# Optimization experiments

Measured on AMD Instinct MI355X. Metric: run time of the kernel, lower is better.

## Reference

```python
import jax, jax.numpy as jnp
import numpy as np

NH = 16      # num_heads
EPS = 1e-6   # RMSNorm eps


def rmsnorm(x, w):
    return x * jax.lax.rsqrt(jnp.mean(x * x, axis=-1, keepdims=True) + EPS) * w


def rotate_half(x):
    x1, x2 = jnp.split(x, 2, axis=-1)
    return jnp.concatenate([-x2, x1], axis=-1)


def apply_rope(x, cos, sin):
    # x: [B,H,N,hd]; cos/sin: [N,hd]
    return x * cos + rotate_half(x) * sin


def attention(x, qkv_w, qkv_b, qn_w, kn_w, proj_w, proj_b, cos, sin):
    B, N, C = x.shape
    hd = C // NH
    qkv = (x @ qkv_w.T + qkv_b).reshape(B, N, 3, NH, hd).transpose(2, 0, 3, 1, 4)
    q, k, v = qkv[0], qkv[1], qkv[2]            # [B,H,N,hd]
    q = apply_rope(rmsnorm(q, qn_w), cos, sin)
    k = apply_rope(rmsnorm(k, kn_w), cos, sin)
    scores = jnp.einsum('bhqd,bhkd->bhqk', q, k) / jnp.sqrt(jnp.float32(hd))
    attn = jax.nn.softmax(scores, axis=-1)
    out = jnp.einsum('bhqk,bhkd->bhqd', attn, v)
    out = out.transpose(0, 2, 1, 3).reshape(B, N, C)
    return out @ proj_w.T + proj_b


def jit_block(x, c, cos_s, sin_s, cos_t, sin_t,
              norm1_w, norm2_w, norm3_w,
              qkv_s_w, qkv_s_b, qn_s_w, kn_s_w, proj_s_w, proj_s_b,
              qkv_t_w, qkv_t_b, qn_t_w, kn_t_w, proj_t_w, proj_t_b,
              w12_w, w12_b, w3_w, w3_b, ada_w, ada_b):
    B, T, L, D = x.shape
    mods = (jax.nn.silu(c) @ ada_w.T + ada_b).reshape(B, 9, D)
    sh_s, sc_s, g_s = mods[:, 0], mods[:, 1], mods[:, 2]
    sh_t, sc_t, g_t = mods[:, 3], mods[:, 4], mods[:, 5]
    sh_m, sc_m, g_m = mods[:, 6], mods[:, 7], mods[:, 8]

    # spatial attention over L, batched over B*T
    xs = x.reshape(B * T, L, D)
    sh = jnp.repeat(sh_s, T, axis=0)
    sc = jnp.repeat(sc_s, T, axis=0)
    g = jnp.repeat(g_s, T, axis=0)
    xs_n = rmsnorm(xs, norm1_w) * (1 + sc[:, None, :]) + sh[:, None, :]
    xs = xs + g[:, None, :] * attention(xs_n, qkv_s_w, qkv_s_b, qn_s_w, kn_s_w,
                                        proj_s_w, proj_s_b, cos_s, sin_s)
    x = xs.reshape(B, T, L, D)

    # temporal attention over T, batched over B*L
    xt = x.transpose(0, 2, 1, 3).reshape(B * L, T, D)
    sh = jnp.repeat(sh_t, L, axis=0)
    sc = jnp.repeat(sc_t, L, axis=0)
    g = jnp.repeat(g_t, L, axis=0)
    xt_n = rmsnorm(xt, norm2_w) * (1 + sc[:, None, :]) + sh[:, None, :]
    xt = xt + g[:, None, :] * attention(xt_n, qkv_t_w, qkv_t_b, qn_t_w, kn_t_w,
                                        proj_t_w, proj_t_b, cos_t, sin_t)
    x = xt.reshape(B, L, T, D).transpose(0, 2, 1, 3)

    # SwiGLU FFN with adaLN modulation + gate
    x_n = rmsnorm(x, norm3_w) * (1 + sc_m[:, None, None, :]) + sh_m[:, None, None, :]
    h12 = x_n @ w12_w.T + w12_b
    h1, h2 = jnp.split(h12, 2, axis=-1)
    mlp_out = (jax.nn.silu(h1) * h2) @ w3_w.T + w3_b
    return x + g_m[:, None, None, :] * mlp_out


def _rope_tables(n, hd):
    inv = 1.0 / (10000.0 ** (np.arange(0, hd, 2, dtype=np.float64) / hd))
    ang = np.arange(n, dtype=np.float64)[:, None] * inv[None, :]
    cos = np.concatenate([np.cos(ang), np.cos(ang)], -1).astype(np.float32)
    sin = np.concatenate([np.sin(ang), np.sin(ang)], -1).astype(np.float32)
    return jnp.asarray(cos), jnp.asarray(sin)


def setup_inputs() -> dict:
    key = jax.random.key(0)
    B, T, L, D = 2, 16, 256, 1024
    HD = D // NH
    HFF = int(int(D * 4.0) * 2 / 3)  # 2730
    ks = jax.random.split(key, 16)
    s = 0.02
    cos_s, sin_s = _rope_tables(L, HD)
    cos_t, sin_t = _rope_tables(T, HD)
    return {
        'x': jax.random.normal(ks[0], (B, T, L, D), jnp.float32),
        'c': jax.random.normal(ks[1], (B, D), jnp.float32),
        'cos_s': cos_s, 'sin_s': sin_s, 'cos_t': cos_t, 'sin_t': sin_t,
        'norm1_w': jnp.ones((D,), jnp.float32),
        'norm2_w': jnp.ones((D,), jnp.float32),
        'norm3_w': jnp.ones((D,), jnp.float32),
        'qkv_s_w': jax.random.normal(ks[2], (3 * D, D), jnp.float32) * s,
        'qkv_s_b': jnp.zeros((3 * D,), jnp.float32),
        'qn_s_w': jnp.ones((HD,), jnp.float32),
        'kn_s_w': jnp.ones((HD,), jnp.float32),
        'proj_s_w': jax.random.normal(ks[3], (D, D), jnp.float32) * s,
        'proj_s_b': jnp.zeros((D,), jnp.float32),
        'qkv_t_w': jax.random.normal(ks[4], (3 * D, D), jnp.float32) * s,
        'qkv_t_b': jnp.zeros((3 * D,), jnp.float32),
        'qn_t_w': jnp.ones((HD,), jnp.float32),
        'kn_t_w': jnp.ones((HD,), jnp.float32),
        'proj_t_w': jax.random.normal(ks[5], (D, D), jnp.float32) * s,
        'proj_t_b': jnp.zeros((D,), jnp.float32),
        'w12_w': jax.random.normal(ks[6], (2 * HFF, D), jnp.float32) * s,
        'w12_b': jnp.zeros((2 * HFF,), jnp.float32),
        'w3_w': jax.random.normal(ks[7], (D, HFF), jnp.float32) * s,
        'w3_b': jnp.zeros((D,), jnp.float32),
        'ada_w': jax.random.normal(ks[8], (9 * D, D), jnp.float32) * s,
        'ada_b': jnp.zeros((9 * D,), jnp.float32),
    }


def reference(x, c, cos_s, sin_s, cos_t, sin_t,
              norm1_w, norm2_w, norm3_w,
              qkv_s_w, qkv_s_b, qn_s_w, kn_s_w, proj_s_w, proj_s_b,
              qkv_t_w, qkv_t_b, qn_t_w, kn_t_w, proj_t_w, proj_t_b,
              w12_w, w12_b, w3_w, w3_b, ada_w, ada_b):
    return jit_block(x, c, cos_s, sin_s, cos_t, sin_t,
                     norm1_w, norm2_w, norm3_w,
                     qkv_s_w, qkv_s_b, qn_s_w, kn_s_w, proj_s_w, proj_s_b,
                     qkv_t_w, qkv_t_b, qn_t_w, kn_t_w, proj_t_w, proj_t_b,
                     w12_w, w12_b, w3_w, w3_b, ada_w, ada_b)
```

## Files before the change

kernel.cpp:

```cpp
#include <hip/hip_runtime.h>
#include <cstdint>
#include <cstddef>

typedef unsigned short u16;
typedef __attribute__((ext_vector_type(8))) short short8;
typedef __attribute__((ext_vector_type(4))) float f32x4;

__device__ __forceinline__ float bf2f(u16 u) {
  union { uint32_t u; float f; } x; x.u = ((uint32_t)u) << 16; return x.f;
}
__device__ __forceinline__ u16 f2bf(float f) {
  union { float f; uint32_t u; } x; x.f = f;
  uint32_t r = x.u + 0x7FFFu + ((x.u >> 16) & 1u);
  return (u16)(r >> 16);
}
__device__ __forceinline__ float silu_f(float x) { return x / (1.f + __expf(-x)); }

__device__ __forceinline__ void glds16(const u16* g, u16* l) {
  __builtin_amdgcn_global_load_lds(
      (const __attribute__((address_space(1))) void*)g,
      (__attribute__((address_space(3))) void*)l, 16, 0, 0);
}

#define MFMA16 __builtin_amdgcn_mfma_f32_16x16x32_bf16

__device__ __forceinline__ void wg_barrier() {
  __builtin_amdgcn_sched_barrier(0);
  asm volatile("" ::: "memory");
  __builtin_amdgcn_s_barrier();
  asm volatile("" ::: "memory");
  __builtin_amdgcn_sched_barrier(0);
}

__device__ __forceinline__ void swizzle_mn(int nx, int& mt, int& nt) {
  int bid = blockIdx.y * nx + blockIdx.x;
  int xcd = bid & 7, l = bid >> 3;
  nt = l >> 3;
  mt = (xcd << 3) | (l & 7);
}

__global__ void cvt_pad_kernel(const float* __restrict__ in, u16* __restrict__ out,
                               int cols_out, int rows_in, int cols_in, int row_off, int total) {
  int i = blockIdx.x * 256 + threadIdx.x;
  if (i >= total) return;
  int r = i / cols_out, ci = i - r * cols_out;
  float v = 0.f;
  if (r < rows_in && ci < cols_in) v = in[(size_t)(r + row_off) * cols_in + ci];
  out[i] = f2bf(v);
}

__global__ void mods_kernel(const float* __restrict__ c, const float* __restrict__ ada_w,
                            const float* __restrict__ ada_b, float* __restrict__ mods) {
  int j = blockIdx.x * 4 + (threadIdx.x >> 6);
  int lane = threadIdx.x & 63;
  float a0 = 0.f, a1 = 0.f;
  for (int k = lane; k < 1024; k += 64) {
    float w = ada_w[(size_t)j * 1024 + k];
    a0 += silu_f(c[k]) * w;
    a1 += silu_f(c[1024 + k]) * w;
  }
  #pragma unroll
  for (int off = 32; off > 0; off >>= 1) { a0 += __shfl_down(a0, off); a1 += __shfl_down(a1, off); }
  if (lane == 0) {
    float bb = ada_b[j];
    mods[j] = a0 + bb;
    mods[9216 + j] = a1 + bb;
  }
}

__global__ __launch_bounds__(256) void norm_mod_kernel(
    const float* __restrict__ X, u16* __restrict__ Y,
    const float* __restrict__ nw, const float* __restrict__ mods,
    int sh_idx, int transpose) {
  int row = blockIdx.x;
  int b = row >> 12;
  int in_row;
  if (transpose) { int rem = row & 4095; int l = rem >> 4, t = rem & 15; in_row = (b << 12) + (t << 8) + l; }
  else in_row = row;
  int tid = threadIdx.x;
  float4 v = ((const float4*)(X + (size_t)in_row * 1024))[tid];
  float ss = v.x * v.x + v.y * v.y + v.z * v.z + v.w * v.w;
  #pragma unroll
  for (int off = 32; off > 0; off >>= 1) ss += __shfl_down(ss, off);
  __shared__ float red[4];
  if ((tid & 63) == 0) red[tid >> 6] = ss;
  __syncthreads();
  float rms = rsqrtf((red[0] + red[1] + red[2] + red[3]) * (1.f / 1024.f) + 1e-6f);
  const float* mb = mods + (size_t)b * 9216 + (size_t)sh_idx * 1024;
  float4 sh = ((const float4*)mb)[tid];
  float4 sc = ((const float4*)(mb + 1024))[tid];
  float4 w  = ((const float4*)nw)[tid];
  ushort4 o;
  o.x = f2bf(v.x * rms * w.x * (1.f + sc.x) + sh.x);
  o.y = f2bf(v.y * rms * w.y * (1.f + sc.y) + sh.y);
  o.z = f2bf(v.z * rms * w.z * (1.f + sc.z) + sh.z);
  o.w = f2bf(v.w * rms * w.w * (1.f + sc.w) + sh.w);
  ((ushort4*)(Y + (size_t)row * 1024))[tid] = o;
}

#define CHK2(b, s) (((b) * 4 + (s)) << 13)

__device__ __forceinline__ void stage_half(const u16* __restrict__ gp, int ldk,
                                           int row_base, int k0,
                                           u16* Sbase, int slot_u16,
                                           int wid, int srow, int scol) {
  #pragma unroll
  for (int c = 0; c < 2; c++) {
    int row = c * 64 + wid * 8 + srow;
    glds16(gp + (size_t)(row_base + row) * ldk + (k0 + scol),
           Sbase + slot_u16 + c * 4096 + wid * 512);
  }
}

template<int STORE_BF16>
__global__ __launch_bounds__(512, 2) void gemm256_bt(
    const u16* __restrict__ A, const u16* __restrict__ W,
    const float* __restrict__ bias, void* __restrict__ Cv,
    int K, int ldc) {
  __shared__ u16 S[65536];
  const int tid = threadIdx.x, wid = tid >> 6, lane = tid & 63;
  const int wm = wid >> 2, wn = wid & 3;
  const int quad = lane >> 4, r = lane & 15;
  const int bid = blockIdx.x, xcd = bid & 7, l = bid >> 3;
  const int mt = (xcd << 2) | (l & 3), nt = l >> 2;
  const int m0 = mt * 256, n0 = nt * 256;

  const int srow = lane >> 3;
  const int scol = ((lane & 7) ^ srow) << 3;
  const int kx0 = (quad * 8) ^ ((r & 7) << 3);
  const int kx1 = (32 + quad * 8) ^ ((r & 7) << 3);
  const int arow = (wm * 64 + r) * 64;
  const int brow = (wn * 32 + r) * 64;

  f32x4 zero = {0.f, 0.f, 0.f, 0.f};
  f32x4 acc[8][4];
  #pragma unroll
  for (int i = 0; i < 8; i++)
    #pragma unroll
    for (int j = 0; j < 4; j++) acc[i][j] = zero;
  short8 fA[4][2], fB0[2][2], fB1[2][2];

  const int nk = K >> 6;

  stage_half(A, K, m0,       0, S, CHK2(0,0), wid, srow, scol);
  stage_half(A, K, m0 + 128, 0, S, CHK2(0,1), wid, srow, scol);
  stage_half(W, K, n0,       0, S, CHK2(0,2), wid, srow, scol);
  stage_half(W, K, n0 + 128, 0, S, CHK2(0,3), wid, srow, scol);
  if (nk > 1) {
    stage_half(A, K, m0,       64, S, CHK2(1,0), wid, srow, scol);
    stage_half(W, K, n0 + 128, 64, S, CHK2(1,3), wid, srow, scol);
    asm volatile("s_waitcnt vmcnt(4)" ::: "memory");
  } else {
    asm volatile("s_waitcnt vmcnt(0)" ::: "memory");
  }
  __builtin_amdgcn_s_barrier();

  for (int u = 0; u < nk; ++u) {
    const int cur = u & 1, nxt = cur ^ 1;
    const int k1 = (u + 1) << 6, k2 = (u + 2) << 6;
    const int s1 = (u + 1 < nk), s2 = (u + 2 < nk);
    const u16* cA0 = S + CHK2(cur, 0);
    const u16* cA1 = S + CHK2(cur, 1);
    const u16* cB0 = S + CHK2(cur, 2);
    const u16* cB1 = S + CHK2(cur, 3);

    #pragma unroll
    for (int f = 0; f < 4; f++) {
      fA[f][0] = *(const short8*)(cA0 + arow + f * 1024 + kx0);
      fA[f][1] = *(const short8*)(cA0 + arow + f * 1024 + kx1);
    }
    #pragma unroll
    for (int j = 0; j < 2; j++) {
      fB0[j][0] = *(const short8*)(cB0 + brow + j * 1024 + kx0);
      fB0[j][1] = *(const short8*)(cB0 + brow + j * 1024 + kx1);
    }
    if (s1) stage_half(A, K, m0 + 128, k1, S, CHK2(nxt,1), wid, srow, scol);
    wg_barrier();
    __builtin_amdgcn_s_setprio(1);
    #pragma unroll
    for (int f = 0; f < 4; f++)
      #pragma unroll
      for (int j = 0; j < 2; j++) {
        acc[f][j] = MFMA16(fA[f][0], fB0[j][0], acc[f][j], 0, 0, 0);
        acc[f][j] = MFMA16(fA[f][1], fB0[j][1], acc[f][j], 0, 0, 0);
      }
    __builtin_amdgcn_s_setprio(0);
    wg_barrier();

    #pragma unroll
    for (int j = 0; j < 2; j++) {
      fB1[j][0] = *(const short8*)(cB1 + brow + j * 1024 + kx0);
      fB1[j][1] = *(const short8*)(cB1 + brow + j * 1024 + kx1);
    }
    if (s1) stage_half(W, K, n0, k1, S, CHK2(nxt,2), wid, srow, scol);
    wg_barrier();
    __builtin_amdgcn_s_setprio(1);
    #pragma unroll
    for (int f = 0; f < 4; f++)
      #pragma unroll
      for (int j = 0; j < 2; j++) {
        acc[f][2 + j] = MFMA16(fA[f][0], fB1[j][0], acc[f][2 + j], 0, 0, 0);
        acc[f][2 + j] = MFMA16(fA[f][1], fB1[j][1], acc[f][2 + j], 0, 0, 0);
      }
    __builtin_amdgcn_s_setprio(0);
    wg_barrier();

    #pragma unroll
    for (int f = 0; f < 4; f++) {
      fA[f][0] = *(const short8*)(cA1 + arow + f * 1024 + kx0);
      fA[f][1] = *(const short8*)(cA1 + arow + f * 1024 + kx1);
    }
    if (s2) stage_half(A, K, m0, k2, S, CHK2(cur,0), wid, srow, scol);
    wg_barrier();
    __builtin_amdgcn_s_setprio(1);
    #pragma unroll
    for (int f = 0; f < 4; f++)
      #pragma unroll
      for (int j = 0; j < 2; j++) {
        acc[4 + f][2 + j] = MFMA16(fA[f][0], fB1[j][0], acc[4 + f][2 + j], 0, 0, 0);
        acc[4 + f][2 + j] = MFMA16(fA[f][1], fB1[j][1], acc[4 + f][2 + j], 0, 0, 0);
      }
    __builtin_amdgcn_s_setprio(0);
    wg_barrier();

    if (s2) stage_half(W, K, n0 + 128, k2, S, CHK2(cur,3), wid, srow, scol);
    wg_barrier();
    __builtin_amdgcn_s_setprio(1);
    #pragma unroll
    for (int f = 0; f < 4; f++)
      #pragma unroll
      for (int j = 0; j < 2; j++) {
        acc[4 + f][j] = MFMA16(fA[f][0], fB0[j][0], acc[4 + f][j], 0, 0, 0);
        acc[4 + f][j] = MFMA16(fA[f][1], fB0[j][1], acc[4 + f][j], 0, 0, 0);
      }
    __builtin_amdgcn_s_setprio(0);
    __builtin_amdgcn_sched_barrier(0);
    if (s2)      asm volatile("s_waitcnt vmcnt(4)" ::: "memory");
    else if (s1) asm volatile("s_waitcnt vmcnt(0)" ::: "memory");
    wg_barrier();
  }

  float* Cf = (float*)Cv;
  u16* Ch = (u16*)Cv;
  #pragma unroll
  for (int f = 0; f < 8; f++) {
    int row = m0 + (f >> 2) * 128 + wm * 64 + (f & 3) * 16 + quad * 4;
    #pragma unroll
    for (int j = 0; j < 4; j++) {
      int col = n0 + (j >> 1) * 128 + wn * 32 + (j & 1) * 16 + r;
      float bv = bias[col];
      #pragma unroll
      for (int rr = 0; rr < 4; rr++) {
        float vv = acc[f][j][rr] + bv;
        if (STORE_BF16) Ch[(size_t)(row + rr) * ldc + col] = f2bf(vv);
        else            Cf[(size_t)(row + rr) * ldc + col] = vv;
      }
    }
  }
}

__global__ __launch_bounds__(512, 2) void gemm256_w12(
    const u16* __restrict__ A, const u16* __restrict__ W1, const u16* __restrict__ W2,
    const float* __restrict__ bias, u16* __restrict__ Hb) {
  __shared__ u16 S[65536];
  const int tid = threadIdx.x, wid = tid >> 6, lane = tid & 63;
  const int wm = wid >> 2, wn = wid & 3;
  const int quad = lane >> 4, r = lane & 15;
  const int bid = blockIdx.x, xcd = bid & 7, l = bid >> 3;
  const int mt = (xcd << 2) | (l & 3), nt = l >> 2;
  const int m0 = mt * 256, n0 = nt * 128;

  const int srow = lane >> 3;
  const int scol = ((lane & 7) ^ srow) << 3;
  const int kx0 = (quad * 8) ^ ((r & 7) << 3);
  const int kx1 = (32 + quad * 8) ^ ((r & 7) << 3);
  const int arow = (wm * 64 + r) * 64;
  const int brow = (wn * 32 + r) * 64;
  const int K = 1024, nk = 16;

  f32x4 zero = {0.f, 0.f, 0.f, 0.f};
  f32x4 acc1[8][2], acc2[8][2];
  #pragma unroll
  for (int i = 0; i < 8; i++)
    #pragma unroll
    for (int j = 0; j < 2; j++) { acc1[i][j] = zero; acc2[i][j] = zero; }
  short8 fA[4][2], fW1[2][2], fW2[2][2];

  stage_half(A,  K, m0,       0, S, CHK2(0,0), wid, srow, scol);
  stage_half(A,  K, m0 + 128, 0, S, CHK2(0,1), wid, srow, scol);
  stage_half(W1, K, n0,       0, S, CHK2(0,2), wid, srow, scol);
  stage_half(W2, K, n0,       0, S, CHK2(0,3), wid, srow, scol);
  stage_half(A,  K, m0,      64, S, CHK2(1,0), wid, srow, scol);
  stage_half(W2, K, n0,      64, S, CHK2(1,3), wid, srow, scol);
  asm volatile("s_waitcnt vmcnt(4)" ::: "memory");
  __builtin_amdgcn_s_barrier();

  for (int u = 0; u < nk; ++u) {
    const int cur = u & 1, nxt = cur ^ 1;
    const int k1 = (u + 1) << 6, k2 = (u + 2) << 6;
    const int s1 = (u + 1 < nk), s2 = (u + 2 < nk);
    const u16* cA0 = S + CHK2(cur, 0);
    const u16* cA1 = S + CHK2(cur, 1);
    const u16* cW1 = S + CHK2(cur, 2);
    const u16* cW2 = S + CHK2(cur, 3);

    #pragma unroll
    for (int f = 0; f < 4; f++) {
      fA[f][0] = *(const short8*)(cA0 + arow + f * 1024 + kx0);
      fA[f][1] = *(const short8*)(cA0 + arow + f * 1024 + kx1);
    }
    #pragma unroll
    for (int j = 0; j < 2; j++) {
      fW1[j][0] = *(const short8*)(cW1 + brow + j * 1024 + kx0);
      fW1[j][1] = *(const short8*)(cW1 + brow + j * 1024 + kx1);
    }
    if (s1) stage_half(A, K, m0 + 128, k1, S, CHK2(nxt,1), wid, srow, scol);
    wg_barrier();
    __builtin_amdgcn_s_setprio(1);
    #pragma unroll
    for (int f = 0; f < 4; f++)
      #pragma unroll
      for (int j = 0; j < 2; j++) {
        acc1[f][j] = MFMA16(fA[f][0], fW1[j][0], acc1[f][j], 0, 0, 0);
        acc1[f][j] = MFMA16(fA[f][1], fW1[j][1], acc1[f][j], 0, 0, 0);
      }
    __builtin_amdgcn_s_setprio(0);
    wg_barrier();

    #pragma unroll
    for (int j = 0; j < 2; j++) {
      fW2[j][0] = *(const short8*)(cW2 + brow + j * 1024 + kx0);
      fW2[j][1] = *(const short8*)(cW2 + brow + j * 1024 + kx1);
    }
    if (s1) stage_half(W1, K, n0, k1, S, CHK2(nxt,2), wid, srow, scol);
    wg_barrier();
    __builtin_amdgcn_s_setprio(1);
    #pragma unroll
    for (int f = 0; f < 4; f++)
      #pragma unroll
      for (int j = 0; j < 2; j++) {
        acc2[f][j] = MFMA16(fA[f][0], fW2[j][0], acc2[f][j], 0, 0, 0);
        acc2[f][j] = MFMA16(fA[f][1], fW2[j][1], acc2[f][j], 0, 0, 0);
      }
    __builtin_amdgcn_s_setprio(0);
    wg_barrier();

    #pragma unroll
    for (int f = 0; f < 4; f++) {
      fA[f][0] = *(const short8*)(cA1 + arow + f * 1024 + kx0);
      fA[f][1] = *(const short8*)(cA1 + arow + f * 1024 + kx1);
    }
    if (s2) stage_half(A, K, m0, k2, S, CHK2(cur,0), wid, srow, scol);
    wg_barrier();
    __builtin_amdgcn_s_setprio(1);
    #pragma unroll
    for (int f = 0; f < 4; f++)
      #pragma unroll
      for (int j = 0; j < 2; j++) {
        acc2[4 + f][j] = MFMA16(fA[f][0], fW2[j][0], acc2[4 + f][j], 0, 0, 0);
        acc2[4 + f][j] = MFMA16(fA[f][1], fW2[j][1], acc2[4 + f][j], 0, 0, 0);
      }
    __builtin_amdgcn_s_setprio(0);
    wg_barrier();

    if (s2) stage_half(W2, K, n0, k2, S, CHK2(cur,3), wid, srow, scol);
    wg_barrier();
    __builtin_amdgcn_s_setprio(1);
    #pragma unroll
    for (int f = 0; f < 4; f++)
      #pragma unroll
      for (int j = 0; j < 2; j++) {
        acc1[4 + f][j] = MFMA16(fA[f][0], fW1[j][0], acc1[4 + f][j], 0, 0, 0);
        acc1[4 + f][j] = MFMA16(fA[f][1], fW1[j][1], acc1[4 + f][j], 0, 0, 0);
      }
    __builtin_amdgcn_s_setprio(0);
    __builtin_amdgcn_sched_barrier(0);
    if (s2)      asm volatile("s_waitcnt vmcnt(4)" ::: "memory");
    else if (s1) asm volatile("s_waitcnt vmcnt(0)" ::: "memory");
    wg_barrier();
  }

  #pragma unroll
  for (int f = 0; f < 8; f++) {
    int row = m0 + (f >> 2) * 128 + wm * 64 + (f & 3) * 16 + quad * 4;
    #pragma unroll
    for (int j = 0; j < 2; j++) {
      int col = n0 + wn * 32 + j * 16 + r;
      float b1 = (col < 2730) ? bias[col] : 0.f;
      float b2 = (col < 2730) ? bias[2730 + col] : 0.f;
      #pragma unroll
      for (int rr = 0; rr < 4; rr++) {
        float h1 = acc1[f][j][rr] + b1;
        float h2 = acc2[f][j][rr] + b2;
        Hb[(size_t)(row + rr) * 2816 + col] = f2bf(silu_f(h1) * h2);
      }
    }
  }
}

template<int STORE_BF16>
__global__ __launch_bounds__(256) void gemm_bt(
    const u16* __restrict__ A, const u16* __restrict__ W,
    const float* __restrict__ bias, void* __restrict__ Cv,
    int N, int K, int ldc) {
  __shared__ u16 As[128 * 32];
  __shared__ u16 Bs[128 * 32];
  int tid = threadIdx.x;
  int wid = tid >> 6, lane = tid & 63;
  int quad = lane >> 4, r = lane & 15;
  int mt, nt; swizzle_mn(gridDim.x, mt, nt);
  int m0 = mt * 128, n0 = nt * 128;
  int wm = (wid >> 1) * 64, wn = (wid & 1) * 64;
  int crow = lane >> 2, ccol = (lane & 3) * 8;

  f32x4 zero = {0.f, 0.f, 0.f, 0.f};
  f32x4 acc[4][4];
  #pragma unroll
  for (int i = 0; i < 4; i++)
    #pragma unroll
    for (int j = 0; j < 4; j++) acc[i][j] = zero;

  for (int k0 = 0; k0 < K; k0 += 32) {
    #pragma unroll
    for (int half = 0; half < 2; half++) {
      int chunk = wid + half * 4;
      int row = chunk * 16 + crow;
      glds16(A + (size_t)(m0 + row) * K + k0 + ccol, As + chunk * 512);
      glds16(W + (size_t)(n0 + row) * K + k0 + ccol, Bs + chunk * 512);
    }
    __syncthreads();
    short8 afr[4], bfr[4];
    #pragma unroll
    for (int i = 0; i < 4; i++) afr[i] = *(const short8*)(As + (wm + i * 16 + r) * 32 + quad * 8);
    #pragma unroll
    for (int j = 0; j < 4; j++) bfr[j] = *(const short8*)(Bs + (wn + j * 16 + r) * 32 + quad * 8);
    #pragma unroll
    for (int i = 0; i < 4; i++)
      #pragma unroll
      for (int j = 0; j < 4; j++)
        acc[i][j] = MFMA16(afr[i], bfr[j], acc[i][j], 0, 0, 0);
    __syncthreads();
  }

  float* Cf = (float*)Cv;
  u16* Ch = (u16*)Cv;
  #pragma unroll
  for (int i = 0; i < 4; i++) {
    #pragma unroll
    for (int j = 0; j < 4; j++) {
      int col = n0 + wn + j * 16 + r;
      float bv = bias[col];
      #pragma unroll
      for (int rr = 0; rr < 4; rr++) {
        int row = m0 + wm + i * 16 + quad * 4 + rr;
        float vv = acc[i][j][rr] + bv;
        if (STORE_BF16) Ch[(size_t)row * ldc + col] = f2bf(vv);
        else            Cf[(size_t)row * ldc + col] = vv;
      }
    }
  }
}

#define KSS 72
#define VSS 264
#define PSS 40
__global__ __launch_bounds__(256) void attn_s_mfma(
    const u16* __restrict__ QKV,
    const float* __restrict__ qn_w, const float* __restrict__ kn_w,
    const float* __restrict__ cosT, const float* __restrict__ sinT,
    u16* __restrict__ AO) {
  __shared__ u16 Ks[256 * KSS];
  __shared__ u16 Vt[64 * VSS];
  __shared__ u16 Pl[4 * 32 * PSS];
  int pair = blockIdx.x;
  int s = pair >> 4, h = pair & 15;
  int qhalf = blockIdx.y;
  int tid = threadIdx.x, wid = tid >> 6, lane = tid & 63;
  int quad = lane >> 4, r = lane & 15;

  {
    int j = tid;
    size_t rowb = ((size_t)(s * 256 + j)) * 3072 + (size_t)h * 64;
    const short8* kr = (const short8*)(QKV + rowb + 1024);
    float xk[64]; float ssq = 0.f;
    #pragma unroll
    for (int cg = 0; cg < 8; cg++) {
      short8 kk = kr[cg];
      #pragma unroll
      for (int e = 0; e < 8; e++) { float v = bf2f((u16)kk[e]); xk[cg * 8 + e] = v; ssq += v * v; }
    }
    float rms = rsqrtf(ssq * (1.f / 64.f) + 1e-6f);
    short8 kq[8];
    #pragma unroll
    for (int d = 0; d < 32; d++) {
      float a = xk[d] * rms * kn_w[d];
      float b2 = xk[d + 32] * rms * kn_w[d + 32];
      u16 o0 = f2bf(a * cosT[j * 64 + d] - b2 * sinT[j * 64 + d]);
      u16 o1 = f2bf(b2 * cosT[j * 64 + 32 + d] + a * sinT[j * 64 + 32 + d]);
      kq[d >> 3][d & 7] = (short)o0;
      kq[(d + 32) >> 3][d & 7] = (short)o1;
    }
    #pragma unroll
    for (int cg = 0; cg < 8; cg++) *(short8*)(Ks + j * KSS + cg * 8) = kq[cg];
    const short8* vr = (const short8*)(QKV + rowb + 2048);
    #pragma unroll
    for (int cg = 0; cg < 8; cg++) {
      short8 vv = vr[cg];
      #pragma unroll
      for (int e = 0; e < 8; e++) Vt[(cg * 8 + e) * VSS + j] = (u16)vv[e];
    }
  }

  int qbase = qhalf * 128 + wid * 32;
  short8 qa[2][2];
  float lrow[2][4];
  {
    float qv[2][2][8];
    float ssq[2] = {0.f, 0.f};
    #pragma unroll
    for (int i = 0; i < 2; i++) {
      int grow = s * 256 + qbase + i * 16 + r;
      #pragma unroll
      for (int kk = 0; kk < 2; kk++) {
        short8 qraw = *(const short8*)(QKV + (size_t)grow * 3072 + h * 64 + kk * 32 + quad * 8);
        #pragma unroll
        for (int e = 0; e < 8; e++) { float v = bf2f((u16)qraw[e]); qv[i][kk][e] = v; ssq[i] += v * v; }
      }
    }
    #pragma unroll
    for (int i = 0; i < 2; i++) {
      float sv = ssq[i];
      sv += __shfl_xor(sv, 16);
      sv += __shfl_xor(sv, 32);
      float rms = rsqrtf(sv * (1.f / 64.f) + 1e-6f);
      int qrow = qbase + i * 16 + r;
      #pragma unroll
      for (int e = 0; e < 8; e++) {
        int d0 = quad * 8 + e;
        float a = qv[i][0][e] * rms * qn_w[d0];
        float b2 = qv[i][1][e] * rms * qn_w[d0 + 32];
        qa[i][0][e] = (short)f2bf(a * cosT[qrow * 64 + d0] - b2 * sinT[qrow * 64 + d0]);
        qa[i][1][e] = (short)f2bf(b2 * cosT[qrow * 64 + 32 + d0] + a * sinT[qrow * 64 + 32 + d0]);
      }
    }
  }
  __syncthreads();

  f32x4 zero = {0.f, 0.f, 0.f, 0.f};
  f32x4 acc[2][16];
  #pragma unroll
  for (int i = 0; i < 2; i++)
    #pragma unroll
    for (int j = 0; j < 16; j++) acc[i][j] = zero;
  #pragma unroll
  for (int kk = 0; kk < 2; kk++) {
    #pragma unroll
    for (int j = 0; j < 16; j++) {
      short8 bfr = *(const short8*)(Ks + (j * 16 + r) * KSS + kk * 32 + quad * 8);
      acc[0][j] = MFMA16(qa[0][kk], bfr, acc[0][j], 0, 0, 0);
      acc[1][j] = MFMA16(qa[1][kk], bfr, acc[1][j], 0, 0, 0);
    }
  }

  #pragma unroll
  for (int i = 0; i < 2; i++) {
    #pragma unroll
    for (int rr = 0; rr < 4; rr++) {
      float mx = acc[i][0][rr];
      #pragma unroll
      for (int j = 1; j < 16; j++) mx = fmaxf(mx, acc[i][j][rr]);
      #pragma unroll
      for (int msk = 1; msk < 16; msk <<= 1) mx = fmaxf(mx, __shfl_xor(mx, msk));
      float ls = 0.f;
      #pragma unroll
      for (int j = 0; j < 16; j++) { float p = __expf((acc[i][j][rr] - mx) * 0.125f); acc[i][j][rr] = p; ls += p; }
      #pragma unroll
      for (int msk = 1; msk < 16; msk <<= 1) ls += __shfl_xor(ls, msk);
      lrow[i][rr] = ls;
    }
  }

  f32x4 oacc[2][4];
  #pragma unroll
  for (int i = 0; i < 2; i++)
    #pragma unroll
    for (int j = 0; j < 4; j++) oacc[i][j] = zero;
  u16* plw = Pl + wid * 32 * PSS;
  #pragma unroll
  for (int kk = 0; kk < 8; kk++) {
    #pragma unroll
    for (int i = 0; i < 2; i++)
      #pragma unroll
      for (int jj = 0; jj < 2; jj++) {
        int j = kk * 2 + jj;
        #pragma unroll
        for (int rr = 0; rr < 4; rr++)
          plw[(i * 16 + quad * 4 + rr) * PSS + jj * 16 + r] = f2bf(acc[i][j][rr]);
      }
    short8 pa0 = *(const short8*)(plw + r * PSS + quad * 8);
    short8 pa1 = *(const short8*)(plw + (16 + r) * PSS + quad * 8);
    #pragma unroll
    for (int j4 = 0; j4 < 4; j4++) {
      short8 vfr = *(const short8*)(Vt + (j4 * 16 + r) * VSS + kk * 32 + quad * 8);
      oacc[0][j4] = MFMA16(pa0, vfr, oacc[0][j4], 0, 0, 0);
      oacc[1][j4] = MFMA16(pa1, vfr, oacc[1][j4], 0, 0, 0);
    }
  }

  #pragma unroll
  for (int i = 0; i < 2; i++) {
    #pragma unroll
    for (int rr = 0; rr < 4; rr++) {
      float inv = 1.f / lrow[i][rr];
      int row = s * 256 + qbase + i * 16 + quad * 4 + rr;
      #pragma unroll
      for (int j4 = 0; j4 < 4; j4++)
        AO[(size_t)row * 1024 + h * 64 + j4 * 16 + r] = f2bf(oacc[i][j4][rr] * inv);
    }
  }
}

__global__ __launch_bounds__(256) void attn_t_kernel(
    const u16* __restrict__ QKV,
    const float* __restrict__ qn_w, const float* __restrict__ kn_w,
    const float* __restrict__ cosT, const float* __restrict__ sinT,
    u16* __restrict__ AO) {
  __shared__ u16 kb[256 * 64];
  __shared__ u16 vb[256 * 64];
  int bl = blockIdx.x;
  int tid = threadIdx.x;
  int h = tid >> 4, t = tid & 15;
  size_t rowbase = ((size_t)(bl * 16 + t)) * 3072;
  int slot = h * 16 + t;
  {
    const u16* kr = QKV + rowbase + 1024 + h * 64;
    float xk[64]; float ss = 0.f;
    #pragma unroll
    for (int d = 0; d < 64; d++) { xk[d] = bf2f(kr[d]); ss += xk[d] * xk[d]; }
    float rms = rsqrtf(ss * (1.f / 64.f) + 1e-6f);
    #pragma unroll
    for (int d = 0; d < 64; d++) xk[d] *= rms * kn_w[d];
    #pragma unroll
    for (int d = 0; d < 32; d++) {
      float a = xk[d], bb = xk[d + 32];
      kb[slot * 64 + d]      = f2bf(a * cosT[t * 64 + d]       - bb * sinT[t * 64 + d]);
      kb[slot * 64 + 32 + d] = f2bf(bb * cosT[t * 64 + 32 + d] + a * sinT[t * 64 + 32 + d]);
    }
    const u16* vr = QKV + rowbase + 2048 + h * 64;
    #pragma unroll
    for (int d = 0; d < 64; d++) vb[slot * 64 + d] = vr[d];
  }
  float q[64];
  {
    const u16* qr = QKV + rowbase + h * 64;
    float ss = 0.f;
    #pragma unroll
    for (int d = 0; d < 64; d++) { q[d] = bf2f(qr[d]); ss += q[d] * q[d]; }
    float rms = rsqrtf(ss * (1.f / 64.f) + 1e-6f);
    #pragma unroll
    for (int d = 0; d < 64; d++) q[d] *= rms * qn_w[d];
    #pragma unroll
    for (int d = 0; d < 32; d++) {
      float a = q[d], bb = q[d + 32];
      q[d]      = a * cosT[t * 64 + d]       - bb * sinT[t * 64 + d];
      q[d + 32] = bb * cosT[t * 64 + 32 + d] + a * sinT[t * 64 + 32 + d];
    }
  }
  __syncthreads();
  float scv[16]; float mx = -1e30f;
  #pragma unroll
  for (int j = 0; j < 16; j++) {
    float sc = 0.f;
    const short8* krow = (const short8*)(kb + (h * 16 + j) * 64);
    #pragma unroll
    for (int vv = 0; vv < 8; vv++) {
      short8 kk = krow[vv];
      #pragma unroll
      for (int e = 0; e < 8; e++) sc += q[vv * 8 + e] * bf2f((u16)kk[e]);
    }
    scv[j] = sc * 0.125f;
    mx = fmaxf(mx, scv[j]);
  }
  float ssum = 0.f;
  #pragma unroll
  for (int j = 0; j < 16; j++) { scv[j] = __expf(scv[j] - mx); ssum += scv[j]; }
  float inv = 1.f / ssum;
  float o[64];
  #pragma unroll
  for (int d = 0; d < 64; d++) o[d] = 0.f;
  #pragma unroll
  for (int j = 0; j < 16; j++) {
    const short8* vrow = (const short8*)(vb + (h * 16 + j) * 64);
    #pragma unroll
    for (int vv = 0; vv < 8; vv++) {
      short8 vk = vrow[vv];
      #pragma unroll
      for (int e = 0; e < 8; e++) o[vv * 8 + e] += scv[j] * bf2f((u16)vk[e]);
    }
  }
  u16* op = AO + ((size_t)(bl * 16 + t)) * 1024 + h * 64;
  #pragma unroll
  for (int d = 0; d < 64; d++) op[d] = f2bf(o[d] * inv);
}

__global__ void resid_kernel(const float* __restrict__ base, const float* __restrict__ P,
                             const float* __restrict__ mods, int gidx,
                             float* __restrict__ out, int transpose) {
  int e = blockIdx.x * 256 + threadIdx.x;
  int row = e >> 10, d = e & 1023;
  int b = row >> 12;
  float g = mods[(size_t)b * 9216 + (size_t)gidx * 1024 + d];
  float p;
  if (transpose) {
    int rem = row & 4095; int t = rem >> 8, l = rem & 255;
    size_t mp = ((size_t)(b << 12)) + (l << 4) + t;
    p = P[(mp << 10) + d];
  } else p = P[e];
  out[e] = base[e] + g * p;
}

extern "C" void kernel_launch(void* const* d_in, const int* in_sizes, int n_in,
                              void* d_out, int out_size, void* d_ws, size_t ws_size,
                              hipStream_t stream) {
  const float* x        = (const float*)d_in[0];
  const float* c        = (const float*)d_in[1];
  const float* cos_s    = (const float*)d_in[2];
  const float* sin_s    = (const float*)d_in[3];
  const float* cos_t    = (const float*)d_in[4];
  const float* sin_t    = (const float*)d_in[5];
  const float* norm1w   = (const float*)d_in[6];
  const float* norm2w   = (const float*)d_in[7];
  const float* norm3w   = (const float*)d_in[8];
  const float* qkv_s_w  = (const float*)d_in[9];
  const float* qkv_s_b  = (const float*)d_in[10];
  const float* qn_s_w   = (const float*)d_in[11];
  const float* kn_s_w   = (const float*)d_in[12];
  const float* proj_s_w = (const float*)d_in[13];
  const float* proj_s_b = (const float*)d_in[14];
  const float* qkv_t_w  = (const float*)d_in[15];
  const float* qkv_t_b  = (const float*)d_in[16];
  const float* qn_t_w   = (const float*)d_in[17];
  const float* kn_t_w   = (const float*)d_in[18];
  const float* proj_t_w = (const float*)d_in[19];
  const float* proj_t_b = (const float*)d_in[20];
  const float* w12_w    = (const float*)d_in[21];
  const float* w12_b    = (const float*)d_in[22];
  const float* w3_w     = (const float*)d_in[23];
  const float* w3_b     = (const float*)d_in[24];
  const float* ada_w    = (const float*)d_in[25];
  const float* ada_b    = (const float*)d_in[26];
  float* out = (float*)d_out;

  char* wsp = (char*)d_ws;
  size_t off = 0;
  auto alloc = [&](size_t bytes) { size_t p = off; off += (bytes + 255) & ~(size_t)255; return p; };
  float* modsb = (float*)(wsp + alloc(2 * 9216 * 4));
  u16*   BIG   = (u16*)  (wsp + alloc((size_t)8192 * 3072 * 2));
  char*  XnP   = (char*) (wsp + alloc((size_t)8192 * 1024 * 4));
  u16*   AO    = (u16*)  (wsp + alloc((size_t)8192 * 1024 * 2));
  u16*   Wq    = (u16*)  (wsp + alloc((size_t)3072 * 1024 * 2));
  u16*   Wp    = (u16*)  (wsp + alloc((size_t)2816 * 1024 * 2));
  u16*   W3b   = (u16*)  (wsp + alloc((size_t)1024 * 2816 * 2));
  u16* W1p = Wq;
  u16* W2p = Wp;
  u16* Xn  = (u16*)XnP;
  float* P = (float*)XnP;
  float* Xcur = out;

  dim3 blk(256);
  dim3 blk512(512);
  int tot;
  mods_kernel<<<2304, blk, 0, stream>>>(c, ada_w, ada_b, modsb);

  tot = 3072 * 1024; cvt_pad_kernel<<<(tot + 255) / 256, blk, 0, stream>>>(qkv_s_w, Wq, 1024, 3072, 1024, 0, tot);
  tot = 1024 * 1024; cvt_pad_kernel<<<(tot + 255) / 256, blk, 0, stream>>>(proj_s_w, Wp, 1024, 1024, 1024, 0, tot);
  norm_mod_kernel<<<8192, blk, 0, stream>>>(x, Xn, norm1w, modsb, 0, 0);
  gemm256_bt<1><<<dim3(32 * 12), blk512, 0, stream>>>(Xn, Wq, qkv_s_b, BIG, 1024, 3072);
  attn_s_mfma<<<dim3(512, 2), blk, 0, stream>>>(BIG, qn_s_w, kn_s_w, cos_s, sin_s, AO);
  gemm_bt<0><<<dim3(8, 64), blk, 0, stream>>>(AO, Wp, proj_s_b, P, 1024, 1024, 1024);
  resid_kernel<<<32768, blk, 0, stream>>>(x, P, modsb, 2, Xcur, 0);

  tot = 3072 * 1024; cvt_pad_kernel<<<(tot + 255) / 256, blk, 0, stream>>>(qkv_t_w, Wq, 1024, 3072, 1024, 0, tot);
  tot = 1024 * 1024; cvt_pad_kernel<<<(tot + 255) / 256, blk, 0, stream>>>(proj_t_w, Wp, 1024, 1024, 1024, 0, tot);
  norm_mod_kernel<<<8192, blk, 0, stream>>>(Xcur, Xn, norm2w, modsb, 3, 1);
  gemm256_bt<1><<<dim3(32 * 12), blk512, 0, stream>>>(Xn, Wq, qkv_t_b, BIG, 1024, 3072);
  attn_t_kernel<<<512, blk, 0, stream>>>(BIG, qn_t_w, kn_t_w, cos_t, sin_t, AO);
  gemm_bt<0><<<dim3(8, 64), blk, 0, stream>>>(AO, Wp, proj_t_b, P, 1024, 1024, 1024);
  resid_kernel<<<32768, blk, 0, stream>>>(Xcur, P, modsb, 5, Xcur, 1);

  tot = 2816 * 1024; cvt_pad_kernel<<<(tot + 255) / 256, blk, 0, stream>>>(w12_w, W1p, 1024, 2730, 1024, 0, tot);
  tot = 2816 * 1024; cvt_pad_kernel<<<(tot + 255) / 256, blk, 0, stream>>>(w12_w, W2p, 1024, 2730, 1024, 2730, tot);
  tot = 1024 * 2816; cvt_pad_kernel<<<(tot + 255) / 256, blk, 0, stream>>>(w3_w, W3b, 2816, 1024, 2730, 0, tot);
  norm_mod_kernel<<<8192, blk, 0, stream>>>(Xcur, Xn, norm3w, modsb, 6, 0);
  gemm256_w12<<<dim3(32 * 22), blk512, 0, stream>>>(Xn, W1p, W2p, w12_b, BIG);
  gemm_bt<0><<<dim3(8, 64), blk, 0, stream>>>(BIG, W3b, w3_b, P, 1024, 2816, 1024);
  resid_kernel<<<32768, blk, 0, stream>>>(Xcur, P, modsb, 8, out, 0);
}
```

Measured before the change: 787.2 us.

## Fuse gated residual into pipelined 256x128 GEMM for projection and w3

Replaces the simple 128x128 single-buffered gemm_bt plus separate resid_kernel with a new 256x128 double-buffered MFMA GEMM whose epilogue applies the bias, the gated residual add, and the temporal-layout transpose directly. This removes the fp32 intermediate P write and re-read and three elementwise launches, and uses a better-pipelined GEMM for the proj and w3 matmuls. The temporal case reads and writes Xcur in place with permuted rows. That is safe only because each output element is read then written by the same thread.

```diff
diff --git a/kernel.cpp b/kernel.cpp
--- a/kernel.cpp
+++ b/kernel.cpp
@@ -30,13 +30,6 @@
   __builtin_amdgcn_s_barrier();
   asm volatile("" ::: "memory");
   __builtin_amdgcn_sched_barrier(0);
-}
-
-__device__ __forceinline__ void swizzle_mn(int nx, int& mt, int& nt) {
-  int bid = blockIdx.y * nx + blockIdx.x;
-  int xcd = bid & 7, l = bid >> 3;
-  nt = l >> 3;
-  mt = (xcd << 3) | (l & 7);
 }
 
 __global__ void cvt_pad_kernel(const float* __restrict__ in, u16* __restrict__ out,
@@ -99,6 +92,7 @@
 }
 
 #define CHK2(b, s) (((b) * 4 + (s)) << 13)
+#define CHK3(b, s) (((b) * 3 + (s)) << 13)
 
 __device__ __forceinline__ void stage_half(const u16* __restrict__ gp, int ldk,
                                            int row_base, int k0,
@@ -259,6 +253,133 @@
   }
 }
 
+template<int MODE>
+__global__ __launch_bounds__(512, 2) void gemm256_n128(
+    const u16* __restrict__ A, const u16* __restrict__ W,
+    const float* __restrict__ bias, void* __restrict__ Cv,
+    int K, int ldc,
+    const float* __restrict__ base, const float* __restrict__ mods, int gidx) {
+  __shared__ u16 S[49152];
+  const int tid = threadIdx.x, wid = tid >> 6, lane = tid & 63;
+  const int wm = wid >> 2, wn = wid & 3;
+  const int quad = lane >> 4, r = lane & 15;
+  const int bid = blockIdx.x, xcd = bid & 7, l = bid >> 3;
+  const int mt = (xcd << 2) | (l & 3), nt = l >> 2;
+  const int m0 = mt * 256, n0 = nt * 128;
+
+  const int srow = lane >> 3;
+  const int scol = ((lane & 7) ^ srow) << 3;
+  const int kx0 = (quad * 8) ^ ((r & 7) << 3);
+  const int kx1 = (32 + quad * 8) ^ ((r & 7) << 3);
+  const int arow = (wm * 64 + r) * 64;
+  const int brow = (wn * 32 + r) * 64;
+
+  f32x4 zero = {0.f, 0.f, 0.f, 0.f};
+  f32x4 acc[8][2];
+  #pragma unroll
+  for (int i = 0; i < 8; i++)
+    #pragma unroll
+    for (int j = 0; j < 2; j++) acc[i][j] = zero;
+  short8 fA[4][2], fB[2][2];
+
+  const int nk = K >> 6;
+
+  stage_half(A, K, m0,       0, S, CHK3(0,0), wid, srow, scol);
+  stage_half(A, K, m0 + 128, 0, S, CHK3(0,1), wid, srow, scol);
+  stage_half(W, K, n0,       0, S, CHK3(0,2), wid, srow, scol);
+  if (nk > 1) {
+    stage_half(A, K, m0, 64, S, CHK3(1,0), wid, srow, scol);
+    asm volatile("s_waitcnt vmcnt(2)" ::: "memory");
+  } else {
+    asm volatile("s_waitcnt vmcnt(0)" ::: "memory");
+  }
+  __builtin_amdgcn_s_barrier();
+
+  for (int u = 0; u < nk; ++u) {
+    const int cur = u & 1, nxt = cur ^ 1;
+    const int k1 = (u + 1) << 6, k2 = (u + 2) << 6;
+    const int s1 = (u + 1 < nk), s2 = (u + 2 < nk);
+    const u16* cA0 = S + CHK3(cur, 0);
+    const u16* cA1 = S + CHK3(cur, 1);
+    const u16* cB  = S + CHK3(cur, 2);
+
+    #pragma unroll
+    for (int f = 0; f < 4; f++) {
+      fA[f][0] = *(const short8*)(cA0 + arow + f * 1024 + kx0);
+      fA[f][1] = *(const short8*)(cA0 + arow + f * 1024 + kx1);
+    }
+    #pragma unroll
+    for (int j = 0; j < 2; j++) {
+      fB[j][0] = *(const short8*)(cB + brow + j * 1024 + kx0);
+      fB[j][1] = *(const short8*)(cB + brow + j * 1024 + kx1);
+    }
+    if (s1) {
+      stage_half(A, K, m0 + 128, k1, S, CHK3(nxt,1), wid, srow, scol);
+      stage_half(W, K, n0,       k1, S, CHK3(nxt,2), wid, srow, scol);
+    }
+    wg_barrier();
+    __builtin_amdgcn_s_setprio(1);
+    #pragma unroll
+    for (int f = 0; f < 4; f++)
+      #pragma unroll
+      for (int j = 0; j < 2; j++) {
+        acc[f][j] = MFMA16(fA[f][0], fB[j][0], acc[f][j], 0, 0, 0);
+        acc[f][j] = MFMA16(fA[f][1], fB[j][1], acc[f][j], 0, 0, 0);
+      }
+    __builtin_amdgcn_s_setprio(0);
+    wg_barrier();
+
+    #pragma unroll
+    for (int f = 0; f < 4; f++) {
+      fA[f][0] = *(const short8*)(cA1 + arow + f * 1024 + kx0);
+      fA[f][1] = *(const short8*)(cA1 + arow + f * 1024 + kx1);
+    }
+    if (s2) stage_half(A, K, m0, k2, S, CHK3(cur,0), wid, srow, scol);
+    wg_barrier();
+    __builtin_amdgcn_s_setprio(1);
+    #pragma unroll
+    for (int f = 0; f < 4; f++)
+      #pragma unroll
+      for (int j = 0; j < 2; j++) {
+        acc[4 + f][j] = MFMA16(fA[f][0], fB[j][0], acc[4 + f][j], 0, 0, 0);
+        acc[4 + f][j] = MFMA16(fA[f][1], fB[j][1], acc[4 + f][j], 0, 0, 0);
+      }
+    __builtin_amdgcn_s_setprio(0);
+    __builtin_amdgcn_sched_barrier(0);
+    if (s2)      asm volatile("s_waitcnt vmcnt(2)" ::: "memory");
+    else if (s1) asm volatile("s_waitcnt vmcnt(0)" ::: "memory");
+    wg_barrier();
+  }
+
+  float* Cf = (float*)Cv;
+  u16* Ch = (u16*)Cv;
+  #pragma unroll
+  for (int f = 0; f < 8; f++) {
+    int row = m0 + (f >> 2) * 128 + wm * 64 + (f & 3) * 16 + quad * 4;
+    #pragma unroll
+    for (int j = 0; j < 2; j++) {
+      int col = n0 + wn * 32 + j * 16 + r;
+      float bv = bias[col];
+      #pragma unroll
+      for (int rr = 0; rr < 4; rr++) {
+        int ri = row + rr;
+        float vv = acc[f][j][rr] + bv;
+        if (MODE == 0) {
+          Cf[(size_t)ri * ldc + col] = vv;
+        } else if (MODE == 1) {
+          Ch[(size_t)ri * ldc + col] = f2bf(vv);
+        } else {
+          int ro = ri;
+          if (MODE == 3) { int rem = ri & 4095; ro = (ri & ~4095) + ((rem & 15) << 8) + (rem >> 4); }
+          int b = ri >> 12;
+          float g = mods[(size_t)b * 9216 + (size_t)gidx * 1024 + col];
+          Cf[(size_t)ro * 1024 + col] = base[(size_t)ro * 1024 + col] + g * vv;
+        }
+      }
+    }
+  }
+}
+
 __global__ __launch_bounds__(512, 2) void gemm256_w12(
     const u16* __restrict__ A, const u16* __restrict__ W1, const u16* __restrict__ W2,
     const float* __restrict__ bias, u16* __restrict__ Hb) {
@@ -393,69 +514,6 @@
         float h1 = acc1[f][j][rr] + b1;
         float h2 = acc2[f][j][rr] + b2;
         Hb[(size_t)(row + rr) * 2816 + col] = f2bf(silu_f(h1) * h2);
-      }
-    }
-  }
-}
-
-template<int STORE_BF16>
-__global__ __launch_bounds__(256) void gemm_bt(
-    const u16* __restrict__ A, const u16* __restrict__ W,
-    const float* __restrict__ bias, void* __restrict__ Cv,
-    int N, int K, int ldc) {
-  __shared__ u16 As[128 * 32];
-  __shared__ u16 Bs[128 * 32];
-  int tid = threadIdx.x;
-  int wid = tid >> 6, lane = tid & 63;
-  int quad = lane >> 4, r = lane & 15;
-  int mt, nt; swizzle_mn(gridDim.x, mt, nt);
-  int m0 = mt * 128, n0 = nt * 128;
-  int wm = (wid >> 1) * 64, wn = (wid & 1) * 64;
-  int crow = lane >> 2, ccol = (lane & 3) * 8;
-
-  f32x4 zero = {0.f, 0.f, 0.f, 0.f};
-  f32x4 acc[4][4];
-  #pragma unroll
-  for (int i = 0; i < 4; i++)
-    #pragma unroll
-    for (int j = 0; j < 4; j++) acc[i][j] = zero;
-
-  for (int k0 = 0; k0 < K; k0 += 32) {
-    #pragma unroll
-    for (int half = 0; half < 2; half++) {
-      int chunk = wid + half * 4;
-      int row = chunk * 16 + crow;
-      glds16(A + (size_t)(m0 + row) * K + k0 + ccol, As + chunk * 512);
-      glds16(W + (size_t)(n0 + row) * K + k0 + ccol, Bs + chunk * 512);
-    }
-    __syncthreads();
-    short8 afr[4], bfr[4];
-    #pragma unroll
-    for (int i = 0; i < 4; i++) afr[i] = *(const short8*)(As + (wm + i * 16 + r) * 32 + quad * 8);
-    #pragma unroll
-    for (int j = 0; j < 4; j++) bfr[j] = *(const short8*)(Bs + (wn + j * 16 + r) * 32 + quad * 8);
-    #pragma unroll
-    for (int i = 0; i < 4; i++)
-      #pragma unroll
-      for (int j = 0; j < 4; j++)
-        acc[i][j] = MFMA16(afr[i], bfr[j], acc[i][j], 0, 0, 0);
-    __syncthreads();
-  }
-
-  float* Cf = (float*)Cv;
-  u16* Ch = (u16*)Cv;
-  #pragma unroll
-  for (int i = 0; i < 4; i++) {
-    #pragma unroll
-    for (int j = 0; j < 4; j++) {
-      int col = n0 + wn + j * 16 + r;
-      float bv = bias[col];
-      #pragma unroll
-      for (int rr = 0; rr < 4; rr++) {
-        int row = m0 + wm + i * 16 + quad * 4 + rr;
-        float vv = acc[i][j][rr] + bv;
-        if (STORE_BF16) Ch[(size_t)row * ldc + col] = f2bf(vv);
-        else            Cf[(size_t)row * ldc + col] = vv;
       }
     }
   }
@@ -701,22 +759,6 @@
   u16* op = AO + ((size_t)(bl * 16 + t)) * 1024 + h * 64;
   #pragma unroll
   for (int d = 0; d < 64; d++) op[d] = f2bf(o[d] * inv);
-}
-
-__global__ void resid_kernel(const float* __restrict__ base, const float* __restrict__ P,
-                             const float* __restrict__ mods, int gidx,
-                             float* __restrict__ out, int transpose) {
-  int e = blockIdx.x * 256 + threadIdx.x;
-  int row = e >> 10, d = e & 1023;
-  int b = row >> 12;
-  float g = mods[(size_t)b * 9216 + (size_t)gidx * 1024 + d];
-  float p;
-  if (transpose) {
-    int rem = row & 4095; int t = rem >> 8, l = rem & 255;
-    size_t mp = ((size_t)(b << 12)) + (l << 4) + t;
-    p = P[(mp << 10) + d];
-  } else p = P[e];
-  out[e] = base[e] + g * p;
 }
 
 extern "C" void kernel_launch(void* const* d_in, const int* in_sizes, int n_in,
@@ -764,7 +806,6 @@
   u16* W1p = Wq;
   u16* W2p = Wp;
   u16* Xn  = (u16*)XnP;
-  float* P = (float*)XnP;
   float* Xcur = out;
 
   dim3 blk(256);
@@ -777,22 +818,19 @@
   norm_mod_kernel<<<8192, blk, 0, stream>>>(x, Xn, norm1w, modsb, 0, 0);
   gemm256_bt<1><<<dim3(32 * 12), blk512, 0, stream>>>(Xn, Wq, qkv_s_b, BIG, 1024, 3072);
   attn_s_mfma<<<dim3(512, 2), blk, 0, stream>>>(BIG, qn_s_w, kn_s_w, cos_s, sin_s, AO);
-  gemm_bt<0><<<dim3(8, 64), blk, 0, stream>>>(AO, Wp, proj_s_b, P, 1024, 1024, 1024);
-  resid_kernel<<<32768, blk, 0, stream>>>(x, P, modsb, 2, Xcur, 0);
+  gemm256_n128<2><<<dim3(32 * 8), blk512, 0, stream>>>(AO, Wp, proj_s_b, Xcur, 1024, 1024, x, modsb, 2);
 
   tot = 3072 * 1024; cvt_pad_kernel<<<(tot + 255) / 256, blk, 0, stream>>>(qkv_t_w, Wq, 1024, 3072, 1024, 0, tot);
   tot = 1024 * 1024; cvt_pad_kernel<<<(tot + 255) / 256, blk, 0, stream>>>(proj_t_w, Wp, 1024, 1024, 1024, 0, tot);
   norm_mod_kernel<<<8192, blk, 0, stream>>>(Xcur, Xn, norm2w, modsb, 3, 1);
   gemm256_bt<1><<<dim3(32 * 12), blk512, 0, stream>>>(Xn, Wq, qkv_t_b, BIG, 1024, 3072);
   attn_t_kernel<<<512, blk, 0, stream>>>(BIG, qn_t_w, kn_t_w, cos_t, sin_t, AO);
-  gemm_bt<0><<<dim3(8, 64), blk, 0, stream>>>(AO, Wp, proj_t_b, P, 1024, 1024, 1024);
-  resid_kernel<<<32768, blk, 0, stream>>>(Xcur, P, modsb, 5, Xcur, 1);
+  gemm256_n128<3><<<dim3(32 * 8), blk512, 0, stream>>>(AO, Wp, proj_t_b, Xcur, 1024, 1024, Xcur, modsb, 5);
 
   tot = 2816 * 1024; cvt_pad_kernel<<<(tot + 255) / 256, blk, 0, stream>>>(w12_w, W1p, 1024, 2730, 1024, 0, tot);
   tot = 2816 * 1024; cvt_pad_kernel<<<(tot + 255) / 256, blk, 0, stream>>>(w12_w, W2p, 1024, 2730, 1024, 2730, tot);
   tot = 1024 * 2816; cvt_pad_kernel<<<(tot + 255) / 256, blk, 0, stream>>>(w3_w, W3b, 2816, 1024, 2730, 0, tot);
   norm_mod_kernel<<<8192, blk, 0, stream>>>(Xcur, Xn, norm3w, modsb, 6, 0);
   gemm256_w12<<<dim3(32 * 22), blk512, 0, stream>>>(Xn, W1p, W2p, w12_b, BIG);
-  gemm_bt<0><<<dim3(8, 64), blk, 0, stream>>>(BIG, W3b, w3_b, P, 1024, 2816, 1024);
-  resid_kernel<<<32768, blk, 0, stream>>>(Xcur, P, modsb, 8, out, 0);
-}
+  gemm256_n128<2><<<dim3(32 * 8), blk512, 0, stream>>>(BIG, W3b, w3_b, out, 2816, 1024, Xcur, modsb, 8);
+}
```

Result: slower. 827.6 us (+5.1%).
